# Performance work log

Measured on AMD Instinct MI355X. Metric: run time of the kernel, lower is better.

## Reference

```python
import jax, jax.numpy as jnp
import numpy as np

B, S, H, NH = 4, 2048, 1024, 16
HD = H // NH


def setup_inputs() -> dict:
    key = jax.random.key(0)
    ks = jax.random.split(key, 9)
    s = 1.0 / np.sqrt(H)
    return {
        "x": jax.random.normal(ks[0], (B, S, H), dtype=jnp.float32),
        "wq": jax.random.normal(ks[1], (H, H), dtype=jnp.float32) * s,
        "bq": jax.random.normal(ks[2], (H,), dtype=jnp.float32) * 0.02,
        "wk": jax.random.normal(ks[3], (H, H), dtype=jnp.float32) * s,
        "bk": jax.random.normal(ks[4], (H,), dtype=jnp.float32) * 0.02,
        "wv": jax.random.normal(ks[5], (H, H), dtype=jnp.float32) * s,
        "bv": jax.random.normal(ks[6], (H,), dtype=jnp.float32) * 0.02,
        "wo": jax.random.normal(ks[7], (H, H), dtype=jnp.float32) * s,
        "bo": jax.random.normal(ks[8], (H,), dtype=jnp.float32) * 0.02,
    }


def reference(x, wq, bq, wk, bk, wv, bv, wo, bo):
    b, s, h = x.shape
    def heads(t):  # (b,s,h) -> (b,nh,s,hd)
        return t.reshape(b, s, NH, HD).transpose(0, 2, 1, 3)
    q = heads(x @ wq.T + bq)
    k = heads(x @ wk.T + bk)
    v = heads(x @ wv.T + bv)
    scores = jnp.einsum("bnqd,bnkd->bnqk", q, k) / np.sqrt(HD).astype(np.float32)
    causal = jnp.tril(jnp.ones((s, s), dtype=bool))
    scores = jnp.where(causal[None, None], scores, -jnp.inf)
    probs = jax.nn.softmax(scores, axis=-1)
    out = jnp.einsum("bnqk,bnkd->bnqd", probs, v)
    out = out.transpose(0, 2, 1, 3).reshape(b, s, h)
    return out @ wo.T + bo
```

## Files before the change

kernel.cpp:

```cpp
#include <hip/hip_runtime.h>
#include <hip/hip_bf16.h>

using bf16 = __bf16;
typedef __attribute__((ext_vector_type(4))) bf16 bf16x4;
typedef __attribute__((ext_vector_type(8))) bf16 bf16x8;
typedef __attribute__((ext_vector_type(4))) float f32x4;
typedef __attribute__((ext_vector_type(16))) float f32x16;

constexpr int kB = 4, kS = 2048, kH = 1024, kNH = 16, kHD = 64;
constexpr int kM = kB * kS;

__device__ __forceinline__ float exp2a(float x) {
  float r;
  asm("v_exp_f32 %0, %1" : "=v"(r) : "v"(x));
  return r;
}
__device__ __forceinline__ unsigned pk2(float a, float b) {
  unsigned short ua = __builtin_bit_cast(unsigned short, (bf16)a);
  unsigned short ub = __builtin_bit_cast(unsigned short, (bf16)b);
  return (unsigned)ua | ((unsigned)ub << 16);
}
__device__ __forceinline__ void glds16(const bf16* g, bf16* l) {
  __builtin_amdgcn_global_load_lds(
      (const __attribute__((address_space(1))) unsigned*)g,
      (__attribute__((address_space(3))) unsigned*)l, 16, 0, 0);
}

__global__ __launch_bounds__(256) void cvt_all_kernel(
    const float* __restrict__ x, const float* __restrict__ w0,
    const float* __restrict__ w1, const float* __restrict__ w2,
    const float* __restrict__ w3, bf16* __restrict__ xb,
    bf16* __restrict__ wb) {
  const int blk = blockIdx.x;
  const float* src;
  bf16* dst;
  int rel;
  if (blk < kM) {
    src = x; dst = xb; rel = blk;
  } else {
    const int wi = (blk - kM) >> 10;
    rel = (blk - kM) & 1023;
    src = wi == 0 ? w0 : wi == 1 ? w1 : wi == 2 ? w2 : w3;
    dst = wb + (size_t)wi * kH * kH;
  }
  const size_t i = (size_t)rel * 256 + threadIdx.x;
  const float4 f = ((const float4*)src)[i];
  bf16x4 o;
  o[0] = (bf16)f.x; o[1] = (bf16)f.y; o[2] = (bf16)f.z; o[3] = (bf16)f.w;
  ((bf16x4*)dst)[i] = o;
}

template <int MODE>
__device__ __forceinline__ void mm_body(const bf16* __restrict__ A,
                                        const bf16* __restrict__ W,
                                        const float* __restrict__ bias,
                                        void* __restrict__ Cp) {
  __shared__ __align__(16) bf16 As[128 * 32];
  __shared__ __align__(16) bf16 Bs[128 * 32];
  const int tid = threadIdx.x;
  const int lane = tid & 63;
  const int wid = tid >> 6;
  const int wr = wid >> 1, wc = wid & 1;
  const int fr = lane & 15, fg = lane >> 4;
  const int bm = blockIdx.x * 128, bn = blockIdx.y * 128;
  const bf16* Ab = A + (size_t)bm * kH;
  const bf16* Wb = W + (size_t)bn * kH;
  const int srow = lane >> 2;
  const int scol = (lane & 3) * 8;
  const int rb0 = wid * 32, rb1 = wid * 32 + 16;

  f32x4 acc[4][4] = {};

  for (int k0 = 0; k0 < kH; k0 += 32) {
    __syncthreads();
    glds16(Ab + (size_t)(rb0 + srow) * kH + k0 + scol, As + rb0 * 32);
    glds16(Ab + (size_t)(rb1 + srow) * kH + k0 + scol, As + rb1 * 32);
    glds16(Wb + (size_t)(rb0 + srow) * kH + k0 + scol, Bs + rb0 * 32);
    glds16(Wb + (size_t)(rb1 + srow) * kH + k0 + scol, Bs + rb1 * 32);
    __syncthreads();

    bf16x8 af[4], bfv[4];
#pragma unroll
    for (int m = 0; m < 4; ++m)
      af[m] = *(const bf16x8*)(As + (wr * 64 + m * 16 + fr) * 32 + fg * 8);
#pragma unroll
    for (int n = 0; n < 4; ++n)
      bfv[n] = *(const bf16x8*)(Bs + (wc * 64 + n * 16 + fr) * 32 + fg * 8);
#pragma unroll
    for (int m = 0; m < 4; ++m)
#pragma unroll
      for (int n = 0; n < 4; ++n)
        acc[m][n] = __builtin_amdgcn_mfma_f32_16x16x32_bf16(af[m], bfv[n],
                                                            acc[m][n], 0, 0, 0);
  }

#pragma unroll
  for (int n = 0; n < 4; ++n) {
    const int nabs = bn + wc * 64 + n * 16 + fr;
    const float bv = bias[nabs];
#pragma unroll
    for (int m = 0; m < 4; ++m) {
      if (MODE == 2) {
        const int tok0 = bm + wr * 64 + m * 16 + fg * 4;
        const int b = tok0 >> 11, s0 = tok0 & (kS - 1);
        const int h = nabs >> 6, d = nabs & 63;
        bf16x4 pv;
#pragma unroll
        for (int reg = 0; reg < 4; ++reg) pv[reg] = (bf16)(acc[m][n][reg] + bv);
        *(bf16x4*)((bf16*)Cp + (((size_t)(b * kNH + h) * kHD + d) * kS + s0)) = pv;
      } else {
#pragma unroll
        for (int reg = 0; reg < 4; ++reg) {
          const int tok = bm + wr * 64 + m * 16 + fg * 4 + reg;
          const float v = acc[m][n][reg] + bv;
          if (MODE == 0) {
            ((float*)Cp)[(size_t)tok * kH + nabs] = v;
          } else {
            const int b = tok >> 11, s = tok & (kS - 1);
            const int h = nabs >> 6, d = nabs & 63;
            ((bf16*)Cp)[(((size_t)(b * kNH + h)) * kS + s) * kHD + d] = (bf16)v;
          }
        }
      }
    }
  }
}

__global__ __launch_bounds__(256) void qkv_kernel(
    const bf16* __restrict__ xb, const bf16* __restrict__ wb,
    const float* __restrict__ bq, const float* __restrict__ bk,
    const float* __restrict__ bv, bf16* __restrict__ qh,
    bf16* __restrict__ kh, bf16* __restrict__ vh) {
  const int z = blockIdx.z;
  const bf16* W = wb + (size_t)z * kH * kH;
  if (z == 0) mm_body<1>(xb, W, bq, qh);
  else if (z == 1) mm_body<1>(xb, W, bk, kh);
  else mm_body<2>(xb, W, bv, vh);
}

__global__ __launch_bounds__(256) void oproj_kernel(
    const bf16* __restrict__ ab, const bf16* __restrict__ wob,
    const float* __restrict__ bo, float* __restrict__ out) {
  mm_body<0>(ab, wob, bo, out);
}

__global__ __launch_bounds__(256) void attn_kernel(
    const bf16* __restrict__ Qh, const bf16* __restrict__ Kh,
    const bf16* __restrict__ Vt, bf16* __restrict__ Ab) {
  __shared__ __align__(16) bf16 Ks[64 * 64];
  __shared__ __align__(16) bf16 Vs[64 * 64];
  const int tid = threadIdx.x;
  const int lane = tid & 63;
  const int wid = tid >> 6;
  const int l31 = lane & 31;
  const int hi = lane >> 5;
  const int bh = blockIdx.x;
  const int qt = gridDim.y - 1 - blockIdx.y;
  const int b = bh >> 4, h = bh & (kNH - 1);

  const int qfirst = qt * 128 + wid * 32;
  const int qrow = qfirst + l31;

  const bf16* Qg = Qh + (size_t)bh * kS * kHD;
  const bf16* Kg = Kh + (size_t)bh * kS * kHD;
  const bf16* Vg = Vt + (size_t)bh * kHD * kS;

  bf16x8 qf[4];
#pragma unroll
  for (int kb = 0; kb < 4; ++kb)
    qf[kb] = *(const bf16x8*)(Qg + (size_t)qrow * kHD + kb * 16 + hi * 8);

  f32x16 Oa0 = {}, Oa1 = {};
  float mreg = -3.0e38f, lreg = 0.f;
  constexpr float kScale = 0.125f * 1.44269504f;

  const int sr = tid >> 2;
  const int sc = tid & 3;
  const int nt64 = qt * 2 + 2;

  for (int kt = 0; kt < nt64; ++kt) {
    const int kt0 = kt * 64;
    const bf16x8 kr0 = *(const bf16x8*)(Kg + (size_t)(kt0 + sr) * kHD + sc * 8);
    const bf16x8 kr1 = *(const bf16x8*)(Kg + (size_t)(kt0 + sr) * kHD + (sc + 4) * 8);
    const bf16x8 vr0 = *(const bf16x8*)(Vg + (size_t)sr * kS + kt0 + sc * 8);
    const bf16x8 vr1 = *(const bf16x8*)(Vg + (size_t)sr * kS + kt0 + (sc + 4) * 8);
    __syncthreads();
    *(bf16x8*)((char*)Ks + sr * 128 + ((sc ^ (sr & 7)) << 4)) = kr0;
    *(bf16x8*)((char*)Ks + sr * 128 + (((sc + 4) ^ (sr & 7)) << 4)) = kr1;
    *(bf16x8*)((char*)Vs + sr * 128 + ((sc ^ (sr & 7)) << 4)) = vr0;
    *(bf16x8*)((char*)Vs + sr * 128 + (((sc + 4) ^ (sr & 7)) << 4)) = vr1;
    __syncthreads();

#pragma unroll
    for (int st = 0; st < 2; ++st) {
      const int kabs = kt0 + st * 32;
      if (kabs > qfirst) continue;
      const bool diag = (kabs == qfirst);

      f32x16 S = {};
#pragma unroll
      for (int kb = 0; kb < 4; ++kb) {
        const int row = st * 32 + l31;
        const int slot = ((kb * 2 + hi) ^ (row & 7));
        const bf16x8 kf = *(const bf16x8*)((char*)Ks + row * 128 + (slot << 4));
        S = __builtin_amdgcn_mfma_f32_32x32x16_bf16(kf, qf[kb], S, 0, 0, 0);
      }

      float p[16];
      float tm = -3.0e38f;
#pragma unroll
      for (int r = 0; r < 16; ++r) {
        float s2 = S[r] * kScale;
        if (diag) {
          const int key = kabs + (r & 3) + 8 * (r >> 2) + 4 * hi;
          if (key > qrow) s2 = -3.0e38f;
        }
        p[r] = s2;
        tm = fmaxf(tm, s2);
      }
      tm = fmaxf(tm, __shfl_xor(tm, 32, 64));
      const float mnew = fmaxf(mreg, tm);
      const float e = exp2a(mreg - mnew);
      mreg = mnew;
      float ps = 0.f;
#pragma unroll
      for (int r = 0; r < 16; ++r) {
        p[r] = exp2a(p[r] - mnew);
        ps += p[r];
      }
      ps += __shfl_xor(ps, 32, 64);
      lreg = lreg * e + ps;
#pragma unroll
      for (int r = 0; r < 16; ++r) { Oa0[r] *= e; Oa1[r] *= e; }

      bf16x8 pf[2];
#pragma unroll
      for (int kb2 = 0; kb2 < 2; ++kb2) {
        const int o = kb2 * 8;
        unsigned a01 = pk2(p[o + 0], p[o + 1]);
        unsigned a45 = pk2(p[o + 4], p[o + 5]);
        asm("v_permlane32_swap_b32 %0, %1" : "+v"(a01), "+v"(a45));
        unsigned a23 = pk2(p[o + 2], p[o + 3]);
        unsigned a67 = pk2(p[o + 6], p[o + 7]);
        asm("v_permlane32_swap_b32 %0, %1" : "+v"(a23), "+v"(a67));
        union { unsigned u[4]; bf16x8 v; } t;
        t.u[0] = a01; t.u[1] = a23; t.u[2] = a45; t.u[3] = a67;
        pf[kb2] = t.v;
      }

#pragma unroll
      for (int kb2 = 0; kb2 < 2; ++kb2) {
        {
          const int row = l31;
          const int slot = ((st * 4 + kb2 * 2 + hi) ^ (row & 7));
          const bf16x8 vf = *(const bf16x8*)((char*)Vs + row * 128 + (slot << 4));
          Oa0 = __builtin_amdgcn_mfma_f32_32x32x16_bf16(vf, pf[kb2], Oa0, 0, 0, 0);
        }
        {
          const int row = 32 + l31;
          const int slot = ((st * 4 + kb2 * 2 + hi) ^ (row & 7));
          const bf16x8 vf = *(const bf16x8*)((char*)Vs + row * 128 + (slot << 4));
          Oa1 = __builtin_amdgcn_mfma_f32_32x32x16_bf16(vf, pf[kb2], Oa1, 0, 0, 0);
        }
      }
    }
  }

  const float rl = 1.f / lreg;
  bf16* const orow = Ab + ((size_t)b * kS + qrow) * kH + h * 64;
#pragma unroll
  for (int rq = 0; rq < 4; ++rq) {
    bf16x4 o0, o1;
#pragma unroll
    for (int j = 0; j < 4; ++j) {
      o0[j] = (bf16)(Oa0[rq * 4 + j] * rl);
      o1[j] = (bf16)(Oa1[rq * 4 + j] * rl);
    }
    *(bf16x4*)(orow + rq * 8 + hi * 4) = o0;
    *(bf16x4*)(orow + 32 + rq * 8 + hi * 4) = o1;
  }
}

extern "C" void kernel_launch(void* const* d_in, const int* in_sizes, int n_in,
                              void* d_out, int out_size, void* d_ws,
                              size_t ws_size, hipStream_t stream) {
  const float* x = (const float*)d_in[0];
  const float* wq = (const float*)d_in[1];
  const float* bq = (const float*)d_in[2];
  const float* wk = (const float*)d_in[3];
  const float* bk = (const float*)d_in[4];
  const float* wv = (const float*)d_in[5];
  const float* bv = (const float*)d_in[6];
  const float* wo = (const float*)d_in[7];
  const float* bo = (const float*)d_in[8];
  float* out = (float*)d_out;

  const size_t perHead = (size_t)kB * kNH * kS * kHD;
  bf16* xb = (bf16*)d_ws;
  bf16* wb = xb + (size_t)kM * kH;
  bf16* qh = wb + (size_t)4 * kH * kH;
  bf16* kh = qh + perHead;
  bf16* vh = kh + perHead;
  bf16* ab = vh + perHead;

  dim3 blk(256);
  cvt_all_kernel<<<dim3(kM + 4 * 1024), blk, 0, stream>>>(x, wq, wk, wv, wo,
                                                          xb, wb);
  qkv_kernel<<<dim3(kM / 128, kH / 128, 3), blk, 0, stream>>>(
      xb, wb, bq, bk, bv, qh, kh, vh);
  attn_kernel<<<dim3(kB * kNH, kS / 128), blk, 0, stream>>>(qh, kh, vh, ab);
  oproj_kernel<<<dim3(kM / 128, kH / 128), blk, 0, stream>>>(
      ab, wb + (size_t)3 * kH * kH, bo, out);
}
```

Before: 191.2 us.

## Drop LDS staging in attention, fold softmax scale into Q, remap grid

The attention kernel now loads K and V fragments straight from global memory into registers for each 32-key sub-tile, with no shared memory and no block barriers. Each wave iterates only over its own causal range instead of the block-wide range. The softmax scale (1/sqrt(d)·log2e) is folded into the Q projection epilogue, which removes a multiply per score. The grid becomes 1D with an XCD-aware remap so that blocks of the same head land on the same die for L2 reuse. The trade-off is that K/V are no longer shared across the four waves, so global/L2 traffic rises and load latency becomes exposed, and Q is rounded to bf16 after scaling.

```diff
diff --git a/kernel.cpp b/kernel.cpp
--- a/kernel.cpp
+++ b/kernel.cpp
@@ -54,7 +54,7 @@
 __device__ __forceinline__ void mm_body(const bf16* __restrict__ A,
                                         const bf16* __restrict__ W,
                                         const float* __restrict__ bias,
-                                        void* __restrict__ Cp) {
+                                        void* __restrict__ Cp, float scale) {
   __shared__ __align__(16) bf16 As[128 * 32];
   __shared__ __align__(16) bf16 Bs[128 * 32];
   const int tid = threadIdx.x;
@@ -112,7 +112,7 @@
 #pragma unroll
         for (int reg = 0; reg < 4; ++reg) {
           const int tok = bm + wr * 64 + m * 16 + fg * 4 + reg;
-          const float v = acc[m][n][reg] + bv;
+          const float v = (acc[m][n][reg] + bv) * scale;
           if (MODE == 0) {
             ((float*)Cp)[(size_t)tok * kH + nabs] = v;
           } else {
@@ -133,29 +133,29 @@
     bf16* __restrict__ kh, bf16* __restrict__ vh) {
   const int z = blockIdx.z;
   const bf16* W = wb + (size_t)z * kH * kH;
-  if (z == 0) mm_body<1>(xb, W, bq, qh);
-  else if (z == 1) mm_body<1>(xb, W, bk, kh);
-  else mm_body<2>(xb, W, bv, vh);
+  if (z == 0) mm_body<1>(xb, W, bq, qh, 0.125f * 1.44269504f);
+  else if (z == 1) mm_body<1>(xb, W, bk, kh, 1.f);
+  else mm_body<2>(xb, W, bv, vh, 1.f);
 }
 
 __global__ __launch_bounds__(256) void oproj_kernel(
     const bf16* __restrict__ ab, const bf16* __restrict__ wob,
     const float* __restrict__ bo, float* __restrict__ out) {
-  mm_body<0>(ab, wob, bo, out);
+  mm_body<0>(ab, wob, bo, out, 1.f);
 }
 
 __global__ __launch_bounds__(256) void attn_kernel(
     const bf16* __restrict__ Qh, const bf16* __restrict__ Kh,
     const bf16* __restrict__ Vt, bf16* __restrict__ Ab) {
-  __shared__ __align__(16) bf16 Ks[64 * 64];
-  __shared__ __align__(16) bf16 Vs[64 * 64];
   const int tid = threadIdx.x;
   const int lane = tid & 63;
   const int wid = tid >> 6;
   const int l31 = lane & 31;
   const int hi = lane >> 5;
-  const int bh = blockIdx.x;
-  const int qt = gridDim.y - 1 - blockIdx.y;
+  const int orig = blockIdx.x;
+  const int wg = (orig & 7) * 128 + (orig >> 3);
+  const int bh = wg >> 4;
+  const int qt = 15 - (wg & 15);
   const int b = bh >> 4, h = bh & (kNH - 1);
 
   const int qfirst = qt * 128 + wid * 32;
@@ -172,98 +172,78 @@
 
   f32x16 Oa0 = {}, Oa1 = {};
   float mreg = -3.0e38f, lreg = 0.f;
-  constexpr float kScale = 0.125f * 1.44269504f;
-
-  const int sr = tid >> 2;
-  const int sc = tid & 3;
-  const int nt64 = qt * 2 + 2;
-
-  for (int kt = 0; kt < nt64; ++kt) {
-    const int kt0 = kt * 64;
-    const bf16x8 kr0 = *(const bf16x8*)(Kg + (size_t)(kt0 + sr) * kHD + sc * 8);
-    const bf16x8 kr1 = *(const bf16x8*)(Kg + (size_t)(kt0 + sr) * kHD + (sc + 4) * 8);
-    const bf16x8 vr0 = *(const bf16x8*)(Vg + (size_t)sr * kS + kt0 + sc * 8);
-    const bf16x8 vr1 = *(const bf16x8*)(Vg + (size_t)sr * kS + kt0 + (sc + 4) * 8);
-    __syncthreads();
-    *(bf16x8*)((char*)Ks + sr * 128 + ((sc ^ (sr & 7)) << 4)) = kr0;
-    *(bf16x8*)((char*)Ks + sr * 128 + (((sc + 4) ^ (sr & 7)) << 4)) = kr1;
-    *(bf16x8*)((char*)Vs + sr * 128 + ((sc ^ (sr & 7)) << 4)) = vr0;
-    *(bf16x8*)((char*)Vs + sr * 128 + (((sc + 4) ^ (sr & 7)) << 4)) = vr1;
-    __syncthreads();
-
-#pragma unroll
-    for (int st = 0; st < 2; ++st) {
-      const int kabs = kt0 + st * 32;
-      if (kabs > qfirst) continue;
-      const bool diag = (kabs == qfirst);
-
-      f32x16 S = {};
-#pragma unroll
-      for (int kb = 0; kb < 4; ++kb) {
-        const int row = st * 32 + l31;
-        const int slot = ((kb * 2 + hi) ^ (row & 7));
-        const bf16x8 kf = *(const bf16x8*)((char*)Ks + row * 128 + (slot << 4));
-        S = __builtin_amdgcn_mfma_f32_32x32x16_bf16(kf, qf[kb], S, 0, 0, 0);
+
+  const bf16* kp = Kg + (size_t)l31 * kHD;
+  const bf16* vp0 = Vg + (size_t)l31 * kS;
+  const bf16* vp1 = Vg + (size_t)(32 + l31) * kS;
+
+  const int nsub = (qfirst >> 5) + 1;
+  for (int it = 0; it < nsub; ++it) {
+    const int kabs = it * 32;
+    f32x16 S = {};
+#pragma unroll
+    for (int kb = 0; kb < 4; ++kb) {
+      const bf16x8 kf = *(const bf16x8*)(kp + kb * 16 + hi * 8);
+      S = __builtin_amdgcn_mfma_f32_32x32x16_bf16(kf, qf[kb], S, 0, 0, 0);
+    }
+    bf16x8 vf0[2], vf1[2];
+#pragma unroll
+    for (int kb2 = 0; kb2 < 2; ++kb2) {
+      vf0[kb2] = *(const bf16x8*)(vp0 + kabs + kb2 * 16 + hi * 8);
+      vf1[kb2] = *(const bf16x8*)(vp1 + kabs + kb2 * 16 + hi * 8);
+    }
+
+    const bool diag = (it == nsub - 1);
+    float sv[16];
+    float tm = -3.0e38f;
+#pragma unroll
+    for (int r = 0; r < 16; ++r) {
+      float s2 = S[r];
+      if (diag) {
+        const int key = kabs + (r & 3) + 8 * (r >> 2) + 4 * hi;
+        if (key > qrow) s2 = -3.0e38f;
       }
-
-      float p[16];
-      float tm = -3.0e38f;
-#pragma unroll
-      for (int r = 0; r < 16; ++r) {
-        float s2 = S[r] * kScale;
-        if (diag) {
-          const int key = kabs + (r & 3) + 8 * (r >> 2) + 4 * hi;
-          if (key > qrow) s2 = -3.0e38f;
-        }
-        p[r] = s2;
-        tm = fmaxf(tm, s2);
-      }
-      tm = fmaxf(tm, __shfl_xor(tm, 32, 64));
-      const float mnew = fmaxf(mreg, tm);
-      const float e = exp2a(mreg - mnew);
-      mreg = mnew;
-      float ps = 0.f;
-#pragma unroll
-      for (int r = 0; r < 16; ++r) {
-        p[r] = exp2a(p[r] - mnew);
-        ps += p[r];
-      }
-      ps += __shfl_xor(ps, 32, 64);
-      lreg = lreg * e + ps;
-#pragma unroll
-      for (int r = 0; r < 16; ++r) { Oa0[r] *= e; Oa1[r] *= e; }
-
-      bf16x8 pf[2];
-#pragma unroll
-      for (int kb2 = 0; kb2 < 2; ++kb2) {
-        const int o = kb2 * 8;
-        unsigned a01 = pk2(p[o + 0], p[o + 1]);
-        unsigned a45 = pk2(p[o + 4], p[o + 5]);
-        asm("v_permlane32_swap_b32 %0, %1" : "+v"(a01), "+v"(a45));
-        unsigned a23 = pk2(p[o + 2], p[o + 3]);
-        unsigned a67 = pk2(p[o + 6], p[o + 7]);
-        asm("v_permlane32_swap_b32 %0, %1" : "+v"(a23), "+v"(a67));
-        union { unsigned u[4]; bf16x8 v; } t;
-        t.u[0] = a01; t.u[1] = a23; t.u[2] = a45; t.u[3] = a67;
-        pf[kb2] = t.v;
-      }
-
-#pragma unroll
-      for (int kb2 = 0; kb2 < 2; ++kb2) {
-        {
-          const int row = l31;
-          const int slot = ((st * 4 + kb2 * 2 + hi) ^ (row & 7));
-          const bf16x8 vf = *(const bf16x8*)((char*)Vs + row * 128 + (slot << 4));
-          Oa0 = __builtin_amdgcn_mfma_f32_32x32x16_bf16(vf, pf[kb2], Oa0, 0, 0, 0);
-        }
-        {
-          const int row = 32 + l31;
-          const int slot = ((st * 4 + kb2 * 2 + hi) ^ (row & 7));
-          const bf16x8 vf = *(const bf16x8*)((char*)Vs + row * 128 + (slot << 4));
-          Oa1 = __builtin_amdgcn_mfma_f32_32x32x16_bf16(vf, pf[kb2], Oa1, 0, 0, 0);
-        }
-      }
-    }
+      sv[r] = s2;
+      tm = fmaxf(tm, s2);
+    }
+    tm = fmaxf(tm, __shfl_xor(tm, 32, 64));
+    const float mnew = fmaxf(mreg, tm);
+    const float e = exp2a(mreg - mnew);
+    mreg = mnew;
+    float p[16];
+    float ps = 0.f;
+#pragma unroll
+    for (int r = 0; r < 16; ++r) {
+      const float pv = exp2a(sv[r] - mnew);
+      p[r] = pv;
+      ps += pv;
+    }
+    ps += __shfl_xor(ps, 32, 64);
+    lreg = lreg * e + ps;
+#pragma unroll
+    for (int r = 0; r < 16; ++r) { Oa0[r] *= e; Oa1[r] *= e; }
+
+    bf16x8 pf[2];
+#pragma unroll
+    for (int kb2 = 0; kb2 < 2; ++kb2) {
+      const int o = kb2 * 8;
+      unsigned a01 = pk2(p[o + 0], p[o + 1]);
+      unsigned a45 = pk2(p[o + 4], p[o + 5]);
+      asm("v_permlane32_swap_b32 %0, %1" : "+v"(a01), "+v"(a45));
+      unsigned a23 = pk2(p[o + 2], p[o + 3]);
+      unsigned a67 = pk2(p[o + 6], p[o + 7]);
+      asm("v_permlane32_swap_b32 %0, %1" : "+v"(a23), "+v"(a67));
+      union { unsigned u[4]; bf16x8 v; } t;
+      t.u[0] = a01; t.u[1] = a23; t.u[2] = a45; t.u[3] = a67;
+      pf[kb2] = t.v;
+    }
+
+#pragma unroll
+    for (int kb2 = 0; kb2 < 2; ++kb2) {
+      Oa0 = __builtin_amdgcn_mfma_f32_32x32x16_bf16(vf0[kb2], pf[kb2], Oa0, 0, 0, 0);
+      Oa1 = __builtin_amdgcn_mfma_f32_32x32x16_bf16(vf1[kb2], pf[kb2], Oa1, 0, 0, 0);
+    }
+    kp += 32 * kHD;
   }
 
   const float rl = 1.f / lreg;
@@ -308,7 +288,7 @@
                                                           xb, wb);
   qkv_kernel<<<dim3(kM / 128, kH / 128, 3), blk, 0, stream>>>(
       xb, wb, bq, bk, bv, qh, kh, vh);
-  attn_kernel<<<dim3(kB * kNH, kS / 128), blk, 0, stream>>>(qh, kh, vh, ab);
+  attn_kernel<<<dim3(kB * kNH * (kS / 128)), blk, 0, stream>>>(qh, kh, vh, ab);
   oproj_kernel<<<dim3(kM / 128, kH / 128), blk, 0, stream>>>(
       ab, wb + (size_t)3 * kH * kH, bo, out);
 }
```

After: 292.8 us. 53.1% more time.
